# Kernel optimization log

Hardware: AMD Instinct MI355X
Metric: run time of the kernel (lower is better)

Reference implementation:

```python
import jax, jax.numpy as jnp
import numpy as np

B, S, E, H, D = 4, 2048, 1024, 16, 64


def setup_inputs() -> dict:
    key = jax.random.key(0)
    ks = jax.random.split(key, 6)
    scale_in = 1.0 / np.sqrt(E)
    return {
        "x": jax.random.normal(ks[0], (B, S, E), dtype=jnp.float32),
        "Wq": jax.random.normal(ks[1], (H, E, D), dtype=jnp.float32) * scale_in,
        "bq": jnp.zeros((H, D), dtype=jnp.float32),
        "Wk": jax.random.normal(ks[2], (H, E, D), dtype=jnp.float32) * scale_in,
        "bk": jnp.zeros((H, D), dtype=jnp.float32),
        "Wv": jax.random.normal(ks[3], (H, E, D), dtype=jnp.float32) * scale_in,
        "bv": jnp.zeros((H, D), dtype=jnp.float32),
        "Wo": jax.random.normal(ks[4], (H * D, E), dtype=jnp.float32) * (1.0 / np.sqrt(H * D)),
        "bo": jnp.zeros((E,), dtype=jnp.float32),
    }


def reference(x, Wq, bq, Wk, bk, Wv, bv, Wo, bo):
    # Per-head Q/K/V projections, batched over heads: [B,S,E] x [H,E,D] -> [B,H,S,D]
    q = jnp.einsum("bse,hed->bhsd", x, Wq) + bq[None, :, None, :]
    k = jnp.einsum("bse,hed->bhsd", x, Wk) + bk[None, :, None, :]
    v = jnp.einsum("bse,hed->bhsd", x, Wv) + bv[None, :, None, :]

    d = q.shape[-1]
    scores = jnp.einsum("bhqd,bhkd->bhqk", q, k) / jnp.sqrt(jnp.asarray(d, q.dtype))
    # Causal mask (registered tril buffer of size max_seq_len in HeadAttention)
    seq = scores.shape[-1]
    causal = jnp.tril(jnp.ones((seq, seq), dtype=bool))
    scores = jnp.where(causal[None, None, :, :], scores, jnp.asarray(-1e9, scores.dtype))
    attn = jax.nn.softmax(scores, axis=-1)
    out = jnp.einsum("bhqk,bhkd->bhqd", attn, v)  # [B,H,S,D]

    # Concat heads: [B,S,H*D], then output projection (dropout is identity in eval)
    out = out.transpose(0, 2, 1, 3).reshape(out.shape[0], out.shape[2], -1)
    return out @ Wo + bo
```

## Files before the change

kernel.cpp:

```cpp
#include <hip/hip_runtime.h>

typedef __bf16 bf16x8 __attribute__((ext_vector_type(8)));
typedef __bf16 bf16x4 __attribute__((ext_vector_type(4)));
typedef float  f32x4  __attribute__((ext_vector_type(4)));

#define B_    4
#define S_    2048
#define E_    1024
#define H_    16
#define D_    64
#define MROWS (B_*S_)
#define HD3   3072

#define SCORE_SCALE 0.18033688011112043f

__device__ __forceinline__ void load_lds16(const void* g, void* l) {
  __builtin_amdgcn_global_load_lds((__attribute__((address_space(1))) void*)g,
                                   (__attribute__((address_space(3))) void*)l,
                                   16, 0, 0);
}

__device__ __forceinline__ f32x4 mfma16(bf16x8 a, bf16x8 b, f32x4 c) {
  return __builtin_amdgcn_mfma_f32_16x16x32_bf16(a, b, c, 0, 0, 0);
}

__device__ __forceinline__ int swz(int row, int dchunk) {
  return row * 64 + ((dchunk ^ (row & 7)) * 8);
}


__global__ void prep(const float4* __restrict__ x, const float* __restrict__ Wq,
                     const float* __restrict__ Wk, const float* __restrict__ Wv,
                     const float* __restrict__ bq, const float* __restrict__ bk,
                     const float* __restrict__ bv, const float* __restrict__ Wo,
                     __bf16* __restrict__ xb, __bf16* __restrict__ Wt,
                     float* __restrict__ bqkv, __bf16* __restrict__ Wot) {
  __shared__ float t[64][65];
  int bid = blockIdx.x;
  if (bid < 8192) {
    int id = bid * 256 + threadIdx.x;
    float4 v = x[id];
    bf16x4 o = { (__bf16)v.x, (__bf16)v.y, (__bf16)v.z, (__bf16)v.w };
    *(bf16x4*)(xb + 4 * (size_t)id) = o;
    return;
  }
  int tx = threadIdx.x & 63;
  int ty = threadIdx.x >> 6;
  if (bid < 8960) {
    int b2 = bid - 8192;
    int e0 = (b2 & 15) * 64;
    int h  = (b2 >> 4) & 15;
    int p  = b2 >> 8;
    const float* W    = (p == 0) ? Wq : (p == 1) ? Wk : Wv;
    const float* bsrc = (p == 0) ? bq : (p == 1) ? bk : bv;
#pragma unroll
    for (int r = 0; r < 16; ++r) {
      int eL = ty + r * 4;
      t[eL][tx] = W[((size_t)h * 1024 + (e0 + eL)) * 64 + tx];
    }
    __syncthreads();
#pragma unroll
    for (int r = 0; r < 16; ++r) {
      int d = ty + r * 4;
      Wt[((size_t)(p * 1024 + h * 64 + d)) * 1024 + e0 + tx] = (__bf16)t[tx][d];
    }
    if ((b2 & 15) == 0 && threadIdx.x < 64)
      bqkv[p * 1024 + h * 64 + threadIdx.x] = bsrc[h * 64 + threadIdx.x];
  } else {
    int b2 = bid - 8960;
    int hd0 = (b2 >> 4) * 64;
    int e0  = (b2 & 15) * 64;
#pragma unroll
    for (int r = 0; r < 16; ++r) {
      int hdL = ty + r * 4;
      t[hdL][tx] = Wo[(size_t)(hd0 + hdL) * 1024 + e0 + tx];
    }
    __syncthreads();
#pragma unroll
    for (int r = 0; r < 16; ++r) {
      int eL = ty + r * 4;
      Wot[(size_t)(e0 + eL) * 1024 + hd0 + tx] = (__bf16)t[tx][eL];
    }
  }
}


template <int MODE>
__global__ __launch_bounds__(256) void gemm_bt(const __bf16* __restrict__ A,
                                               const __bf16* __restrict__ Bt,
                                               const float* __restrict__ bias,
                                               void* __restrict__ Cout,
                                               __bf16* __restrict__ VT,
                                               int M, int N, int K) {
  __shared__ __attribute__((aligned(16))) __bf16 As[128 * 64];
  __shared__ __attribute__((aligned(16))) __bf16 Bs[128 * 64];
  int tid = threadIdx.x, wave = tid >> 6, lane = tid & 63;
  int quad = lane >> 4, cc = lane & 15;
  int nb = N >> 7;
  int bm = (int)blockIdx.x / nb, bn = (int)blockIdx.x % nb;
  const __bf16* Abase = A + (size_t)bm * 128 * K;
  const __bf16* Bbase = Bt + (size_t)bn * 128 * K;
  int wr = (wave >> 1) * 64, wc = (wave & 1) * 64;
  f32x4 acc[4][4];
#pragma unroll
  for (int i = 0; i < 4; ++i)
#pragma unroll
    for (int j = 0; j < 4; ++j) acc[i][j] = (f32x4){0.f, 0.f, 0.f, 0.f};

  int srow[4], scol[4];
#pragma unroll
  for (int p = 0; p < 4; ++p) {
    int g = tid + p * 256;
    srow[p] = g >> 3;
    scol[p] = ((g & 7) ^ (srow[p] & 7)) * 8;
  }
#pragma unroll
  for (int p = 0; p < 4; ++p) {
    load_lds16(Abase + (size_t)srow[p] * K + scol[p], &As[(tid + p * 256) * 8]);
    load_lds16(Bbase + (size_t)srow[p] * K + scol[p], &Bs[(tid + p * 256) * 8]);
  }

  for (int k0 = 0; k0 < K; k0 += 64) {
    __syncthreads();
    bf16x8 af[2][4], bf[2][4];
#pragma unroll
    for (int kk = 0; kk < 2; ++kk) {
#pragma unroll
      for (int i = 0; i < 4; ++i) af[kk][i] = *(const bf16x8*)&As[swz(wr + i * 16 + cc, kk * 4 + quad)];
#pragma unroll
      for (int j = 0; j < 4; ++j) bf[kk][j] = *(const bf16x8*)&Bs[swz(wc + j * 16 + cc, kk * 4 + quad)];
    }
    __syncthreads();
    if (k0 + 64 < K) {
      int kn = k0 + 64;
#pragma unroll
      for (int p = 0; p < 4; ++p) {
        load_lds16(Abase + (size_t)srow[p] * K + kn + scol[p], &As[(tid + p * 256) * 8]);
        load_lds16(Bbase + (size_t)srow[p] * K + kn + scol[p], &Bs[(tid + p * 256) * 8]);
      }
    }
#pragma unroll
    for (int kk = 0; kk < 2; ++kk)
#pragma unroll
      for (int i = 0; i < 4; ++i)
#pragma unroll
        for (int j = 0; j < 4; ++j) acc[i][j] = mfma16(af[kk][i], bf[kk][j], acc[i][j]);
  }

#pragma unroll
  for (int j = 0; j < 4; ++j) {
    int col = bn * 128 + wc + j * 16 + cc;
    float bv = bias[col];
#pragma unroll
    for (int i = 0; i < 4; ++i) {
      int row0 = bm * 128 + wr + i * 16 + quad * 4;
      if (MODE == 0) {
#pragma unroll
        for (int r = 0; r < 4; ++r)
          ((float*)Cout)[(size_t)(row0 + r) * N + col] = acc[i][j][r] + bv;
      } else if (col < 2048) {
        float sc = (col < 1024) ? SCORE_SCALE : 1.0f;
#pragma unroll
        for (int r = 0; r < 4; ++r)
          ((__bf16*)Cout)[(size_t)(row0 + r) * 2048 + col] = (__bf16)((acc[i][j][r] + bv) * sc);
      } else {
        int bh = (row0 >> 11) * 16 + ((col >> 6) & 15);
        int d  = col & 63;
        bf16x4 pk;
#pragma unroll
        for (int r = 0; r < 4; ++r) pk[r] = (__bf16)(acc[i][j][r] + bv);
        *(bf16x4*)&VT[((size_t)(bh * 64 + d)) * 2048 + (row0 & 2047)] = pk;
      }
    }
  }
}


__global__ __launch_bounds__(512, 4) void attn(const __bf16* __restrict__ QKb,
                                               const __bf16* __restrict__ VT,
                                               __bf16* __restrict__ O,
                                               float* __restrict__ PartO,
                                               float* __restrict__ PartL) {
  int bx = blockIdx.x;
  int bh = bx & 63;
  int g  = bx >> 6;
  int qt, par = 0, split = 0;
  switch (g) {
    case 0: qt = 5; break;
    case 1: qt = 4; break;
    case 2: qt = 7; split = 1; break;
    case 3: qt = 7; par = 1; split = 1; break;
    case 4: qt = 3; break;
    case 5: qt = 6; split = 1; break;
    case 6: qt = 6; par = 1; split = 1; break;
    case 7: qt = 2; break;
    case 8: qt = 1; break;
    default: qt = 0; break;
  }
  int h  = bh & 15;
  int b  = bh >> 4;
  int q0 = qt * 256;
  int tid = threadIdx.x, wave = tid >> 6, lane = tid & 63;
  int quad = lane >> 4, c = lane & 15;
  int tstep = split ? 2 : 1;

  __shared__ __attribute__((aligned(16))) __bf16 smem[32768];
  __bf16* Qs = smem;
  __bf16* Ks = smem + 16384;
  __bf16* Vs = smem + 24576;
  __bf16* Ps = smem + wave * 2048;

  int srow = tid >> 3, sx = ((tid & 7) ^ (srow & 7)) * 8;
  const __bf16* Kp = QKb + ((size_t)(b * S_ + par * 64 + srow)) * 2048 + 1024 + h * 64 + sx;
  const __bf16* Vp = VT + (size_t)bh * (64 * 2048) + (size_t)srow * 2048 + par * 64 + sx;
  const int kstep = tstep * 64 * 2048;
  const int vstep = tstep * 64;
  int ldst = tid * 8;

  const __bf16* Qbase = QKb + (size_t)(b * S_ + q0) * 2048 + h * 64;
#pragma unroll
  for (int p = 0; p < 4; ++p) {
    int gg = tid + p * 512;
    int row = gg >> 3, pch = gg & 7;
    load_lds16(Qbase + (size_t)row * 2048 + (pch ^ (row & 7)) * 8, &Qs[gg * 8]);
  }
  load_lds16(Kp, &Ks[ldst]);
  load_lds16(Vp, &Vs[ldst]);
  Kp += kstep; Vp += vstep;
  __syncthreads();

  bf16x8 qf[2][2];
#pragma unroll
  for (int i = 0; i < 2; ++i)
#pragma unroll
    for (int kk = 0; kk < 2; ++kk)
      qf[i][kk] = *(const bf16x8*)&Qs[swz(wave * 32 + i * 16 + c, kk * 4 + quad)];

  int offA[4][2], offW[2][4];
#pragma unroll
  for (int j = 0; j < 4; ++j)
#pragma unroll
    for (int kk = 0; kk < 2; ++kk) offA[j][kk] = swz(j * 16 + c, kk * 4 + quad);
#pragma unroll
  for (int i = 0; i < 2; ++i) {
    int q_l = i * 16 + c;
#pragma unroll
    for (int j = 0; j < 4; ++j) {
      int dch8 = j * 2 + (quad >> 1);
      offW[i][j] = q_l * 64 + ((dch8 ^ (q_l & 7)) * 8) + (quad & 1) * 4;
    }
  }

  const __bf16 one_b = (__bf16)1.0f;
  bf16x8 ones = { one_b, one_b, one_b, one_b, one_b, one_b, one_b, one_b };

  f32x4 acc_o[2][4], acc_l[2];
#pragma unroll
  for (int i = 0; i < 2; ++i) {
    acc_l[i] = (f32x4){0.f, 0.f, 0.f, 0.f};
#pragma unroll
    for (int j = 0; j < 4; ++j) acc_o[i][j] = (f32x4){0.f, 0.f, 0.f, 0.f};
  }

  int qwave = q0 + wave * 32;
  int ntiles = qt * 4 + 4;
  int cur = 0;
  for (int t = par; t < ntiles; t += tstep) {
    if (t + tstep < ntiles) {
      load_lds16(Kp, &Ks[(cur ^ 1) * 4096 + ldst]);
      load_lds16(Vp, &Vs[(cur ^ 1) * 4096 + ldst]);
      Kp += kstep; Vp += vstep;
    }

    int kv0 = t * 64;
    if (kv0 <= qwave + 31) {
      const __bf16* Kc = Ks + cur * 4096;
      const __bf16* Vc = Vs + cur * 4096;

      f32x4 acc_t[2][4];
#pragma unroll
      for (int i = 0; i < 2; ++i)
#pragma unroll
        for (int j = 0; j < 4; ++j) acc_t[i][j] = (f32x4){0.f, 0.f, 0.f, 0.f};
      bf16x8 kf[4][2];
#pragma unroll
      for (int j = 0; j < 4; ++j)
#pragma unroll
        for (int kk = 0; kk < 2; ++kk)
          kf[j][kk] = *(const bf16x8*)&Kc[offA[j][kk]];
#pragma unroll
      for (int i = 0; i < 2; ++i)
#pragma unroll
        for (int j = 0; j < 4; ++j)
#pragma unroll
          for (int kk = 0; kk < 2; ++kk)
            acc_t[i][j] = mfma16(kf[j][kk], qf[i][kk], acc_t[i][j]);

      bool domask = (kv0 + 63 > qwave);
#pragma unroll
      for (int i = 0; i < 2; ++i) {
        int q_g = qwave + i * 16 + c;
#pragma unroll
        for (int j = 0; j < 4; ++j) {
          bf16x4 pk;
#pragma unroll
          for (int r = 0; r < 4; ++r) {
            float p = __builtin_amdgcn_exp2f(acc_t[i][j][r]);
            if (domask) {
              int kv = kv0 + j * 16 + quad * 4 + r;
              p = (kv > q_g) ? 0.f : p;
            }
            pk[r] = (__bf16)p;
          }
          *(bf16x4*)&Ps[offW[i][j]] = pk;
        }
      }

      bf16x8 pf[2][2], vf[4][2];
#pragma unroll
      for (int i = 0; i < 2; ++i)
#pragma unroll
        for (int kk = 0; kk < 2; ++kk)
          pf[i][kk] = *(const bf16x8*)&Ps[offA[i][kk]];
#pragma unroll
      for (int j = 0; j < 4; ++j)
#pragma unroll
        for (int kk = 0; kk < 2; ++kk)
          vf[j][kk] = *(const bf16x8*)&Vc[offA[j][kk]];
#pragma unroll
      for (int i = 0; i < 2; ++i) {
#pragma unroll
        for (int j = 0; j < 4; ++j)
#pragma unroll
          for (int kk = 0; kk < 2; ++kk)
            acc_o[i][j] = mfma16(pf[i][kk], vf[j][kk], acc_o[i][j]);
        acc_l[i] = mfma16(pf[i][0], ones, acc_l[i]);
        acc_l[i] = mfma16(pf[i][1], ones, acc_l[i]);
      }
    }

    __syncthreads();
    cur ^= 1;
  }

  if (!split) {
    __bf16* Obase = O + (size_t)(b * S_ + q0) * 1024 + h * 64;
#pragma unroll
    for (int i = 0; i < 2; ++i)
#pragma unroll
      for (int r = 0; r < 4; ++r) {
        float rl = 1.0f / acc_l[i][r];
        int row = wave * 32 + i * 16 + quad * 4 + r;
#pragma unroll
        for (int j = 0; j < 4; ++j)
          Obase[(size_t)row * 1024 + j * 16 + c] = (__bf16)(acc_o[i][j][r] * rl);
      }
  } else {
    int slot = par * 128 + (7 - qt) * 64 + bh;
    float* PO = PartO + (size_t)slot * (256 * 64);
    float* PL = PartL + (size_t)slot * 256;
#pragma unroll
    for (int i = 0; i < 2; ++i)
#pragma unroll
      for (int r = 0; r < 4; ++r) {
        int row = wave * 32 + i * 16 + quad * 4 + r;
        if (c == 0) PL[row] = acc_l[i][r];
#pragma unroll
        for (int j = 0; j < 4; ++j)
          PO[row * 64 + j * 16 + c] = acc_o[i][j][r];
      }
  }
}

__global__ void merge(const float* __restrict__ PartO, const float* __restrict__ PartL,
                      __bf16* __restrict__ O) {
  int u  = blockIdx.x >> 2;
  int r0 = (blockIdx.x & 3) * 64;
  int qt = 7 - (u >> 6);
  int bh = u & 63;
  int b = bh >> 4, h = bh & 15;
  int q0 = qt * 256;
  int tid = threadIdx.x;
  const float* A0 = PartO + (size_t)u * (256 * 64) + r0 * 64;
  const float* A1 = PartO + (size_t)(128 + u) * (256 * 64) + r0 * 64;
  const float* L0 = PartL + (size_t)u * 256 + r0;
  const float* L1 = PartL + (size_t)(128 + u) * 256 + r0;
#pragma unroll
  for (int it = 0; it < 4; ++it) {
    int e = it * 1024 + tid * 4;
    int row = e >> 6, d = e & 63;
    f32x4 a0 = *(const f32x4*)&A0[e];
    f32x4 a1 = *(const f32x4*)&A1[e];
    float rl = 1.0f / (L0[row] + L1[row]);
    bf16x4 o;
#pragma unroll
    for (int k = 0; k < 4; ++k) o[k] = (__bf16)((a0[k] + a1[k]) * rl);
    *(bf16x4*)&O[(size_t)(b * S_ + q0 + r0 + row) * 1024 + h * 64 + d] = o;
  }
}


extern "C" void kernel_launch(void* const* d_in, const int* in_sizes, int n_in,
                              void* d_out, int out_size, void* d_ws, size_t ws_size,
                              hipStream_t stream) {
  (void)in_sizes; (void)n_in; (void)out_size; (void)ws_size;
  const float* x  = (const float*)d_in[0];
  const float* Wq = (const float*)d_in[1];
  const float* bq = (const float*)d_in[2];
  const float* Wk = (const float*)d_in[3];
  const float* bk = (const float*)d_in[4];
  const float* Wv = (const float*)d_in[5];
  const float* bv = (const float*)d_in[6];
  const float* Wo = (const float*)d_in[7];
  const float* bo = (const float*)d_in[8];

  char* w = (char*)d_ws;
  __bf16* xb   = (__bf16*)(w);
  __bf16* Wt   = (__bf16*)(w + (16ull << 20));
  __bf16* Wot  = (__bf16*)(w + (22ull << 20));
  float*  bqkv = (float*) (w + (24ull << 20));
  __bf16* QKb  = (__bf16*)(w + (25ull << 20));
  __bf16* Ob   = (__bf16*)(w + (57ull << 20));
  __bf16* VT   = (__bf16*)(w + (73ull << 20));
  float* PartO = (float*)(w);
  float* PartL = (float*)(w + (18ull << 20));

  prep   <<<9216, 256, 0, stream>>>((const float4*)x, Wq, Wk, Wv, bq, bk, bv, Wo,
                                    xb, Wt, bqkv, Wot);
  gemm_bt<1><<<dim3((MROWS / 128) * (3072 / 128)), 256, 0, stream>>>(xb, Wt, bqkv, (void*)QKb, VT, MROWS, 3072, 1024);
  attn   <<<640, 512, 0, stream>>>(QKb, VT, Ob, PartO, PartL);
  merge  <<<512, 256, 0, stream>>>(PartO, PartL, Ob);
  gemm_bt<0><<<dim3((MROWS / 128) * (1024 / 128)), 256, 0, stream>>>(Ob, Wot, bo, d_out, nullptr, MROWS, 1024, 1024);
}
```

Measured before the change: 252.6 us.

## Give each attention wave 64 query rows with 4 waves per block

The attention kernel now runs 256 threads per block instead of 512, and each wave handles 64 query rows instead of 32. Each K/V fragment loaded from LDS is reused across four row groups, and the per-block K/V tile loads are split over two passes per thread. The aim is to reduce LDS fragment traffic and K/V loads per unit of work and to halve the per-block barrier cost. In exchange the kernel holds more accumulator registers, runs fewer waves per block, and the causal skip is coarser at 64 rows per wave.

Result: no change. 249.3 us (-1.3%).

```diff
diff --git a/kernel.cpp b/kernel.cpp
--- a/kernel.cpp
+++ b/kernel.cpp
@@ -176,7 +176,7 @@
 }
 
 
-__global__ __launch_bounds__(512, 4) void attn(const __bf16* __restrict__ QKb,
+__global__ __launch_bounds__(256, 2) void attn(const __bf16* __restrict__ QKb,
                                                const __bf16* __restrict__ VT,
                                                __bf16* __restrict__ O,
                                                float* __restrict__ PartO,
@@ -208,41 +208,51 @@
   __bf16* Qs = smem;
   __bf16* Ks = smem + 16384;
   __bf16* Vs = smem + 24576;
-  __bf16* Ps = smem + wave * 2048;
-
-  int srow = tid >> 3, sx = ((tid & 7) ^ (srow & 7)) * 8;
-  const __bf16* Kp = QKb + ((size_t)(b * S_ + par * 64 + srow)) * 2048 + 1024 + h * 64 + sx;
-  const __bf16* Vp = VT + (size_t)bh * (64 * 2048) + (size_t)srow * 2048 + par * 64 + sx;
+  __bf16* Ps = smem + wave * 4096;
+
+  const __bf16* Kp[2];
+  const __bf16* Vp[2];
+  int ldst[2];
+#pragma unroll
+  for (int p = 0; p < 2; ++p) {
+    int gg = tid + p * 256;
+    int srow = gg >> 3, sx = ((gg & 7) ^ (srow & 7)) * 8;
+    Kp[p] = QKb + ((size_t)(b * S_ + par * 64 + srow)) * 2048 + 1024 + h * 64 + sx;
+    Vp[p] = VT + (size_t)bh * (64 * 2048) + (size_t)srow * 2048 + par * 64 + sx;
+    ldst[p] = gg * 8;
+  }
   const int kstep = tstep * 64 * 2048;
   const int vstep = tstep * 64;
-  int ldst = tid * 8;
 
   const __bf16* Qbase = QKb + (size_t)(b * S_ + q0) * 2048 + h * 64;
 #pragma unroll
-  for (int p = 0; p < 4; ++p) {
-    int gg = tid + p * 512;
+  for (int p = 0; p < 8; ++p) {
+    int gg = tid + p * 256;
     int row = gg >> 3, pch = gg & 7;
     load_lds16(Qbase + (size_t)row * 2048 + (pch ^ (row & 7)) * 8, &Qs[gg * 8]);
   }
-  load_lds16(Kp, &Ks[ldst]);
-  load_lds16(Vp, &Vs[ldst]);
-  Kp += kstep; Vp += vstep;
+#pragma unroll
+  for (int p = 0; p < 2; ++p) {
+    load_lds16(Kp[p], &Ks[ldst[p]]);
+    load_lds16(Vp[p], &Vs[ldst[p]]);
+    Kp[p] += kstep; Vp[p] += vstep;
+  }
   __syncthreads();
 
-  bf16x8 qf[2][2];
-#pragma unroll
-  for (int i = 0; i < 2; ++i)
+  bf16x8 qf[4][2];
+#pragma unroll
+  for (int i = 0; i < 4; ++i)
 #pragma unroll
     for (int kk = 0; kk < 2; ++kk)
-      qf[i][kk] = *(const bf16x8*)&Qs[swz(wave * 32 + i * 16 + c, kk * 4 + quad)];
-
-  int offA[4][2], offW[2][4];
+      qf[i][kk] = *(const bf16x8*)&Qs[swz(wave * 64 + i * 16 + c, kk * 4 + quad)];
+
+  int offA[4][2], offW[4][4];
 #pragma unroll
   for (int j = 0; j < 4; ++j)
 #pragma unroll
     for (int kk = 0; kk < 2; ++kk) offA[j][kk] = swz(j * 16 + c, kk * 4 + quad);
 #pragma unroll
-  for (int i = 0; i < 2; ++i) {
+  for (int i = 0; i < 4; ++i) {
     int q_l = i * 16 + c;
 #pragma unroll
     for (int j = 0; j < 4; ++j) {
@@ -254,58 +264,57 @@
   const __bf16 one_b = (__bf16)1.0f;
   bf16x8 ones = { one_b, one_b, one_b, one_b, one_b, one_b, one_b, one_b };
 
-  f32x4 acc_o[2][4], acc_l[2];
-#pragma unroll
-  for (int i = 0; i < 2; ++i) {
+  f32x4 acc_o[4][4], acc_l[4];
+#pragma unroll
+  for (int i = 0; i < 4; ++i) {
     acc_l[i] = (f32x4){0.f, 0.f, 0.f, 0.f};
 #pragma unroll
     for (int j = 0; j < 4; ++j) acc_o[i][j] = (f32x4){0.f, 0.f, 0.f, 0.f};
   }
 
-  int qwave = q0 + wave * 32;
+  int qwave = q0 + wave * 64;
   int ntiles = qt * 4 + 4;
   int cur = 0;
   for (int t = par; t < ntiles; t += tstep) {
     if (t + tstep < ntiles) {
-      load_lds16(Kp, &Ks[(cur ^ 1) * 4096 + ldst]);
-      load_lds16(Vp, &Vs[(cur ^ 1) * 4096 + ldst]);
-      Kp += kstep; Vp += vstep;
+#pragma unroll
+      for (int p = 0; p < 2; ++p) {
+        load_lds16(Kp[p], &Ks[(cur ^ 1) * 4096 + ldst[p]]);
+        load_lds16(Vp[p], &Vs[(cur ^ 1) * 4096 + ldst[p]]);
+        Kp[p] += kstep; Vp[p] += vstep;
+      }
     }
 
     int kv0 = t * 64;
-    if (kv0 <= qwave + 31) {
+    if (kv0 <= qwave + 63) {
       const __bf16* Kc = Ks + cur * 4096;
       const __bf16* Vc = Vs + cur * 4096;
-
-      f32x4 acc_t[2][4];
-#pragma unroll
-      for (int i = 0; i < 2; ++i)
-#pragma unroll
-        for (int j = 0; j < 4; ++j) acc_t[i][j] = (f32x4){0.f, 0.f, 0.f, 0.f};
+      bool domask = (kv0 + 63 > qwave);
+
       bf16x8 kf[4][2];
 #pragma unroll
       for (int j = 0; j < 4; ++j)
 #pragma unroll
         for (int kk = 0; kk < 2; ++kk)
           kf[j][kk] = *(const bf16x8*)&Kc[offA[j][kk]];
-#pragma unroll
-      for (int i = 0; i < 2; ++i)
+
+#pragma unroll
+      for (int i = 0; i < 4; ++i) {
+        f32x4 acc_t[4];
+#pragma unroll
+        for (int j = 0; j < 4; ++j) acc_t[j] = (f32x4){0.f, 0.f, 0.f, 0.f};
 #pragma unroll
         for (int j = 0; j < 4; ++j)
 #pragma unroll
           for (int kk = 0; kk < 2; ++kk)
-            acc_t[i][j] = mfma16(kf[j][kk], qf[i][kk], acc_t[i][j]);
-
-      bool domask = (kv0 + 63 > qwave);
-#pragma unroll
-      for (int i = 0; i < 2; ++i) {
+            acc_t[j] = mfma16(kf[j][kk], qf[i][kk], acc_t[j]);
         int q_g = qwave + i * 16 + c;
 #pragma unroll
         for (int j = 0; j < 4; ++j) {
           bf16x4 pk;
 #pragma unroll
           for (int r = 0; r < 4; ++r) {
-            float p = __builtin_amdgcn_exp2f(acc_t[i][j][r]);
+            float p = __builtin_amdgcn_exp2f(acc_t[j][r]);
             if (domask) {
               int kv = kv0 + j * 16 + quad * 4 + r;
               p = (kv > q_g) ? 0.f : p;
@@ -316,26 +325,25 @@
         }
       }
 
-      bf16x8 pf[2][2], vf[4][2];
-#pragma unroll
-      for (int i = 0; i < 2; ++i)
-#pragma unroll
-        for (int kk = 0; kk < 2; ++kk)
-          pf[i][kk] = *(const bf16x8*)&Ps[offA[i][kk]];
+      bf16x8 vf[4][2];
 #pragma unroll
       for (int j = 0; j < 4; ++j)
 #pragma unroll
         for (int kk = 0; kk < 2; ++kk)
           vf[j][kk] = *(const bf16x8*)&Vc[offA[j][kk]];
 #pragma unroll
-      for (int i = 0; i < 2; ++i) {
+      for (int i = 0; i < 4; ++i) {
+        bf16x8 pf[2];
+#pragma unroll
+        for (int kk = 0; kk < 2; ++kk)
+          pf[kk] = *(const bf16x8*)&Ps[offA[i][kk]];
 #pragma unroll
         for (int j = 0; j < 4; ++j)
 #pragma unroll
           for (int kk = 0; kk < 2; ++kk)
-            acc_o[i][j] = mfma16(pf[i][kk], vf[j][kk], acc_o[i][j]);
-        acc_l[i] = mfma16(pf[i][0], ones, acc_l[i]);
-        acc_l[i] = mfma16(pf[i][1], ones, acc_l[i]);
+            acc_o[i][j] = mfma16(pf[kk], vf[j][kk], acc_o[i][j]);
+        acc_l[i] = mfma16(pf[0], ones, acc_l[i]);
+        acc_l[i] = mfma16(pf[1], ones, acc_l[i]);
       }
     }
 
@@ -346,11 +354,11 @@
   if (!split) {
     __bf16* Obase = O + (size_t)(b * S_ + q0) * 1024 + h * 64;
 #pragma unroll
-    for (int i = 0; i < 2; ++i)
+    for (int i = 0; i < 4; ++i)
 #pragma unroll
       for (int r = 0; r < 4; ++r) {
         float rl = 1.0f / acc_l[i][r];
-        int row = wave * 32 + i * 16 + quad * 4 + r;
+        int row = wave * 64 + i * 16 + quad * 4 + r;
 #pragma unroll
         for (int j = 0; j < 4; ++j)
           Obase[(size_t)row * 1024 + j * 16 + c] = (__bf16)(acc_o[i][j][r] * rl);
@@ -360,10 +368,10 @@
     float* PO = PartO + (size_t)slot * (256 * 64);
     float* PL = PartL + (size_t)slot * 256;
 #pragma unroll
-    for (int i = 0; i < 2; ++i)
+    for (int i = 0; i < 4; ++i)
 #pragma unroll
       for (int r = 0; r < 4; ++r) {
-        int row = wave * 32 + i * 16 + quad * 4 + r;
+        int row = wave * 64 + i * 16 + quad * 4 + r;
         if (c == 0) PL[row] = acc_l[i][r];
 #pragma unroll
         for (int j = 0; j < 4; ++j)
@@ -428,7 +436,7 @@
   prep   <<<9216, 256, 0, stream>>>((const float4*)x, Wq, Wk, Wv, bq, bk, bv, Wo,
                                     xb, Wt, bqkv, Wot);
   gemm_bt<1><<<dim3((MROWS / 128) * (3072 / 128)), 256, 0, stream>>>(xb, Wt, bqkv, (void*)QKb, VT, MROWS, 3072, 1024);
-  attn   <<<640, 512, 0, stream>>>(QKb, VT, Ob, PartO, PartL);
+  attn   <<<640, 256, 0, stream>>>(QKb, VT, Ob, PartO, PartL);
   merge  <<<512, 256, 0, stream>>>(PartO, PartL, Ob);
   gemm_bt<0><<<dim3((MROWS / 128) * (1024 / 128)), 256, 0, stream>>>(Ob, Wot, bo, d_out, nullptr, MROWS, 1024, 1024);
 }
```
